# Optimization experiments

Hardware: AMD Instinct MI355X
Metric: run time of the kernel (lower is better)

Reference implementation:

```python
import jax, jax.numpy as jnp
import numpy as np

B, C, D, L, H, K, S, OUT = 8, 2048, 128, 3, 4, 200, 64, 24
d = D // H  # d_head = 32


def _ln(x, g, b):
    m = x.mean(-1, keepdims=True)
    v = ((x - m) ** 2).mean(-1, keepdims=True)
    return (x - m) / jnp.sqrt(v + 1e-5) * g + b


def _gelu(x):
    return jax.nn.gelu(x, approximate=False)  # torch default exact GELU


def setup_inputs() -> dict:
    key = jax.random.key(0)
    ks = iter(jax.random.split(key, 32))
    def nrm(shape, std=0.02):
        return jax.random.normal(next(ks), shape, jnp.float32) * std
    return {
        "x": jax.random.uniform(next(ks), (B, C), jnp.float32) * 5.0,
        "role_emb": nrm((C, D)),
        "filler_w": nrm((D,), 0.1),
        "qW": nrm((L, D, D), 0.05), "qb": jnp.zeros((L, D)),
        "kW": nrm((L, D, D), 0.05), "kb": jnp.zeros((L, D)),
        "vW": nrm((L, D, D), 0.05), "vb": jnp.zeros((L, D)),
        "oW": nrm((L, D, D), 0.05), "ob": jnp.zeros((L, D)),
        "relW1": nrm((L, 3 * d, d), 0.05), "relb1": jnp.zeros((L, d)),
        "relW2": nrm((L, d), 0.05), "relb2": jnp.zeros((L,)),
        "ln1_g": jnp.ones((L, D)), "ln1_b": jnp.zeros((L, D)),
        "ln2_g": jnp.ones((L, D)), "ln2_b": jnp.zeros((L, D)),
        "ffnW1": nrm((L, D, 4 * D), 0.05), "ffnb1": jnp.zeros((L, 4 * D)),
        "ffnW2": nrm((L, 4 * D, D), 0.05), "ffnb2": jnp.zeros((L, D)),
        "slots": nrm((S, D)),
        "memln_g": jnp.ones((D,)), "memln_b": jnp.zeros((D,)),
        "task_q": nrm((D,)),
        "headW": nrm((D, OUT), 0.05), "headb": jnp.zeros((OUT,)),
        "top_k": K,
    }


def _forward(x, role_emb, filler_w, qW, qb, kW, kb, vW, vb, oW, ob,
             relW1, relb1, relW2, relb2, ln1_g, ln1_b, ln2_g, ln2_b,
             ffnW1, ffnb1, ffnW2, ffnb2, slots, memln_g, memln_b,
             task_q, headW, headb, top_k):
    Bx = x.shape[0]
    x_log = jnp.log1p(jnp.maximum(x, 0.0))
    vals, idx = jax.lax.top_k(x_log, top_k)            # [B,K] top intensities
    roles = role_emb[idx]                              # [B,K,D]
    fillers = _gelu(vals[..., None] * filler_w)        # Linear(1,D,bias=False)+GELU
    b = roles * fillers                                # hadamard binding [B,K,D]
    sc_d = jnp.float32(d) ** 0.5
    for l in range(qW.shape[0]):
        q = (b @ qW[l] + qb[l]).reshape(Bx, -1, H, d).transpose(0, 2, 1, 3)
        k = (b @ kW[l] + kb[l]).reshape(Bx, -1, H, d).transpose(0, 2, 1, 3)
        v = (b @ vW[l] + vb[l]).reshape(Bx, -1, H, d).transpose(0, 2, 1, 3)
        # MLP_rel([q_i || k_j || q_i*k_j]) decomposed over the 3d input blocks
        W1q, W1k, W1i = relW1[l][:d], relW1[l][d:2 * d], relW1[l][2 * d:]
        qt = jnp.einsum('bhie,ef->bhif', q, W1q)       # [B,H,K,d]
        kt = jnp.einsum('bhje,ef->bhjf', k, W1k)       # [B,H,K,d]
        itm = jnp.einsum('bhie,bhje,ef->bhijf', q, k, W1i)  # pairwise [B,H,K,K,d]
        hrel = _gelu(qt[:, :, :, None, :] + kt[:, :, None, :, :] + itm + relb1[l])
        scores = (jnp.einsum('bhijf,f->bhij', hrel, relW2[l]) + relb2[l]) / sc_d
        attn = jax.nn.softmax(scores, axis=-1)
        o = jnp.einsum('bhij,bhjd->bhid', attn, v)
        o = o.transpose(0, 2, 1, 3).reshape(Bx, -1, D) @ oW[l] + ob[l]
        b = _ln(b + o, ln1_g[l], ln1_b[l])
        f = _gelu(b @ ffnW1[l] + ffnb1[l]) @ ffnW2[l] + ffnb2[l]
        b = _ln(b + f, ln2_g[l], ln2_b[l])
    sc_D = jnp.float32(D) ** 0.5
    ra = jax.nn.softmax(jnp.einsum('bcd,d->bc', b, task_q) / sc_D, axis=-1)
    h = jnp.einsum('bc,bcd->bd', ra, b)                # task-query readout
    ma = jax.nn.softmax(jnp.einsum('sd,bcd->bsc', slots, b) / sc_D, axis=-1)
    mem = _ln(jnp.einsum('bsc,bcd->bsd', ma, b).mean(axis=1), memln_g, memln_b)
    return (h + mem) @ headW + headb                   # [B,OUT]


def reference(x, role_emb, filler_w, qW, qb, kW, kb, vW, vb, oW, ob,
              relW1, relb1, relW2, relb2, ln1_g, ln1_b, ln2_g, ln2_b,
              ffnW1, ffnb1, ffnW2, ffnb2, slots, memln_g, memln_b,
              task_q, headW, headb, top_k):
    return _forward(x, role_emb, filler_w, qW, qb, kW, kb, vW, vb, oW, ob,
                    relW1, relb1, relW2, relb2, ln1_g, ln1_b, ln2_g, ln2_b,
                    ffnW1, ffnb1, ffnW2, ffnb2, slots, memln_g, memln_b,
                    task_q, headW, headb, top_k)
```

## Files before the change

kernel.cpp:

```cpp
#include <hip/hip_runtime.h>
#include <math.h>

#define BQ 8
#define CC 2048
#define DDIM 128
#define LLAY 3
#define HH 4
#define KK 200
#define SSLOT 64
#define OUTN 24
#define DH 32

typedef __bf16 bf16_t;
typedef __bf16 bf16x8 __attribute__((ext_vector_type(8)));
typedef float f32x4 __attribute__((ext_vector_type(4)));

__device__ __forceinline__ float fastrcp(float x) {
#if __has_builtin(__builtin_amdgcn_rcpf)
  return __builtin_amdgcn_rcpf(x);
#else
  return 1.0f / x;
#endif
}
__device__ __forceinline__ float fastexp2(float x) {
#if __has_builtin(__builtin_amdgcn_exp2f)
  return __builtin_amdgcn_exp2f(x);
#else
  return exp2f(x);
#endif
}
__device__ __forceinline__ float fgelu2(float x) {
  float s = x * x;
  float inner = fmaf(0.044715f * s, x, x);
  float e = fastexp2(inner * 2.302118610509359f);
  float r = fastrcp(1.f + e);
  return fmaf(-x, r, x);
}
__device__ __forceinline__ float egelu(float x) {
  return 0.5f * x * (1.f + erff(x * 0.7071067811865476f));
}

__global__ __launch_bounds__(256) void prep_kernel(
    const float* __restrict__ qW, const float* __restrict__ kW,
    const float* __restrict__ vW, const float* __restrict__ oW,
    const float* __restrict__ fW1, const float* __restrict__ fW2,
    bf16_t* __restrict__ wtb,
    const float* __restrict__ x, const float* __restrict__ role_emb,
    const float* __restrict__ fw, float* __restrict__ btok,
    bf16_t* __restrict__ btokbf) {
  __shared__ float Ts[64][65];
  __shared__ float svals[KK];
  __shared__ int sidx[KK];
  __shared__ int red[4];
  __shared__ int cnt;
  const int blk = blockIdx.x, tid = threadIdx.x;
  if (blk < 144) {
    const int t = blk;
    const float* src; bf16_t* dst; int N, K, k0, n0;
    if (t < 48) {
      int which = t / 12, rem = t % 12;
      int l = rem >> 2, tt = rem & 3;
      N = 128; K = 128; k0 = (tt >> 1) * 64; n0 = (tt & 1) * 64;
      src = (which == 0 ? qW : which == 1 ? kW : which == 2 ? vW : oW) + l * 16384;
      dst = wtb + which * 49152 + l * 16384;
    } else if (t < 96) {
      int t2 = t - 48, l = t2 >> 4, tt = t2 & 15;
      N = 512; K = 128; k0 = (tt >> 3) * 64; n0 = (tt & 7) * 64;
      src = fW1 + l * 65536;
      dst = wtb + 196608 + l * 65536;
    } else {
      int t3 = t - 96, l = t3 >> 4, tt = t3 & 15;
      N = 128; K = 512; k0 = (tt >> 1) * 64; n0 = (tt & 1) * 64;
      src = fW2 + l * 65536;
      dst = wtb + 393216 + l * 65536;
    }
#pragma unroll
    for (int i = 0; i < 16; ++i) {
      int u = tid + i * 256;
      int r = u >> 6, c = u & 63;
      Ts[r][c] = src[(size_t)(k0 + r) * N + n0 + c];
    }
    __syncthreads();
#pragma unroll
    for (int i = 0; i < 16; ++i) {
      int u = tid + i * 256;
      int rn = u >> 6, ck = u & 63;
      dst[(size_t)(n0 + rn) * K + k0 + ck] = (bf16_t)Ts[ck][rn];
    }
    return;
  }
  const int b = blk - 144;
  float xv[8]; unsigned xb[8];
#pragma unroll
  for (int t = 0; t < 8; t++) {
    float v = x[b * CC + t * 256 + tid];
    xv[t] = v;
    xb[t] = __float_as_uint(v);
  }
  unsigned lo = 0u, hi = 0x7f800000u;
  while (lo < hi) {
    unsigned mid = (lo + hi) >> 1;
    int c = 0;
#pragma unroll
    for (int t = 0; t < 8; t++) c += (xb[t] > mid) ? 1 : 0;
#pragma unroll
    for (int m = 1; m <= 32; m <<= 1) c += __shfl_xor(c, m);
    if ((tid & 63) == 0) red[tid >> 6] = c;
    __syncthreads();
    int ct = red[0] + red[1] + red[2] + red[3];
    __syncthreads();
    if (ct >= KK) lo = mid + 1; else hi = mid;
  }
  const unsigned thr = lo;
  if (tid == 0) cnt = 0;
  __syncthreads();
#pragma unroll
  for (int t = 0; t < 8; t++) {
    if (xb[t] > thr) {
      int p = atomicAdd(&cnt, 1);
      svals[p] = log1pf(xv[t]);
      sidx[p] = t * 256 + tid;
    }
  }
  __syncthreads();
#pragma unroll
  for (int t = 0; t < 8; t++) {
    if (xb[t] == thr) {
      int p = atomicAdd(&cnt, 1);
      if (p < KK) {
        svals[p] = log1pf(xv[t]);
        sidx[p] = t * 256 + tid;
      }
    }
  }
  __syncthreads();
  for (int u = tid; u < KK * DDIM; u += 256) {
    int dd = u & 127, t = u >> 7;
    float v = svals[t];
    float fill = egelu(v * fw[dd]);
    float val = role_emb[(size_t)sidx[t] * DDIM + dd] * fill;
    btok[(size_t)b * KK * DDIM + u] = val;
    btokbf[(size_t)b * KK * DDIM + u] = (bf16_t)val;
  }
}

__global__ __launch_bounds__(256) void qkv_mfma(const bf16_t* __restrict__ A,
    const bf16_t* __restrict__ qWt, const float* __restrict__ qb,
    const bf16_t* __restrict__ kWt, const float* __restrict__ kb,
    const bf16_t* __restrict__ vWt, const float* __restrict__ vb,
    bf16_t* __restrict__ qo, bf16_t* __restrict__ ko, bf16_t* __restrict__ vo) {
  __shared__ __align__(16) bf16_t Alds[32 * 16 * 8];
  __shared__ __align__(16) bf16_t Blds[128 * 16 * 8];
  const int tid = threadIdx.x, m0 = blockIdx.x * 32, z = blockIdx.y;
  const bf16_t* Wt; const float* bias; bf16_t* C;
  if (z == 0) { Wt = qWt; bias = qb; C = qo; }
  else if (z == 1) { Wt = kWt; bias = kb; C = ko; }
  else { Wt = vWt; bias = vb; C = vo; }
#pragma unroll
  for (int it = 0; it < 2; ++it) {
    int u = tid + it * 256;
    int row = u >> 4, kc = u & 15;
    uint4 d = *(const uint4*)(A + (size_t)(m0 + row) * 128 + kc * 8);
    *(uint4*)&Alds[(row * 16 + (kc ^ (row & 7))) * 8] = d;
  }
#pragma unroll
  for (int it = 0; it < 8; ++it) {
    int u = tid + it * 256;
    int col = u >> 4, kcb = u & 15;
    uint4 d = *(const uint4*)(Wt + (size_t)col * 128 + kcb * 8);
    *(uint4*)&Blds[(col * 16 + (kcb ^ (col & 7))) * 8] = d;
  }
  __syncthreads();
  const int w = tid >> 6, lane = tid & 63, fcol = lane & 15, g = lane >> 4;
  const int wr = w & 1, wn = w >> 1;
  f32x4 acc[4];
#pragma unroll
  for (int ni = 0; ni < 4; ++ni) acc[ni] = (f32x4){0.f, 0.f, 0.f, 0.f};
#pragma unroll
  for (int ks = 0; ks < 4; ++ks) {
    const int arow = 16 * wr + fcol;
    bf16x8 a = *(const bf16x8*)&Alds[(arow * 16 + ((ks * 4 + g) ^ (arow & 7))) * 8];
#pragma unroll
    for (int ni = 0; ni < 4; ++ni) {
      const int bcol = wn * 64 + ni * 16 + fcol;
      bf16x8 b = *(const bf16x8*)&Blds[(bcol * 16 + ((ks * 4 + g) ^ (bcol & 7))) * 8];
      acc[ni] = __builtin_amdgcn_mfma_f32_16x16x32_bf16(a, b, acc[ni], 0, 0, 0);
    }
  }
#pragma unroll
  for (int ni = 0; ni < 4; ++ni) {
    const int col = wn * 64 + ni * 16 + fcol;
    const float bv = bias[col];
#pragma unroll
    for (int r = 0; r < 4; ++r) {
      const int row = m0 + 16 * wr + 4 * g + r;
      C[(size_t)row * 128 + col] = (bf16_t)(acc[ni][r] + bv);
    }
  }
}

__global__ __launch_bounds__(512, 4) void rel_attn_mfma(
    const bf16_t* __restrict__ qbf, const bf16_t* __restrict__ kbf,
    const bf16_t* __restrict__ vbf,
    const float* __restrict__ W1g, const float* __restrict__ b1g,
    const float* __restrict__ w2p, bf16_t* __restrict__ o) {
  __shared__ __align__(16) bf16_t ksh[208 * 32];
  __shared__ __align__(16) bf16_t vtsh[32 * 224];
  __shared__ __align__(16) bf16_t psh[8 * 224];
  __shared__ __align__(16) bf16_t W1ki[32 * 66];
  __shared__ __align__(16) bf16_t qsh[8 * 32];
  __shared__ __align__(16) bf16_t qtshb[8 * 32];
  const int tid = threadIdx.x;
  const int bh = blockIdx.y, bb = bh >> 2, h = bh & 3;
  const int i0 = blockIdx.x * 8;
  const bf16_t* kgb = kbf + (size_t)(bb * KK) * DDIM + h * DH;
  const bf16_t* vgb = vbf + (size_t)(bb * KK) * DDIM + h * DH;
  const bf16_t* qgb = qbf + (size_t)(bb * KK) * DDIM + h * DH;
#pragma unroll
  for (int it = 0; it < 2; ++it) {
    int u = tid + it * 512;
    if (u < 832) {
      int j = u >> 2, bi = u & 3;
      uint4 d = {0u, 0u, 0u, 0u};
      if (j < KK) d = *(const uint4*)(kgb + (size_t)j * DDIM + bi * 8);
      *(uint4*)&ksh[j * 32 + (bi ^ ((j >> 1) & 3)) * 8] = d;
    }
  }
#pragma unroll
  for (int it = 0; it < 7; ++it) {
    int u = tid + it * 512;
    if (u < 3328) {
      int jp = u >> 5, f = u & 31;
      int j0 = jp * 2;
      bf16_t a0 = (j0 < KK) ? vgb[(size_t)j0 * DDIM + f] : (bf16_t)0.f;
      bf16_t a1 = (j0 + 1 < KK) ? vgb[(size_t)(j0 + 1) * DDIM + f] : (bf16_t)0.f;
      union { bf16_t h2[2]; unsigned uu; } pk;
      pk.h2[0] = a0; pk.h2[1] = a1;
      *(unsigned*)&vtsh[f * 224 + j0] = pk.uu;
    }
  }
  if (tid < 256) {
    int f = tid >> 3, cp = tid & 7;
    *(unsigned*)&vtsh[f * 224 + 208 + cp * 2] = 0u;
  }
  if (tid < 64) {
    int r = tid >> 3, cp = tid & 7;
    *(unsigned*)&psh[r * 224 + 208 + cp * 2] = 0u;
  }
#pragma unroll
  for (int it = 0; it < 4; ++it) {
    int u = tid + it * 512;
    int sel = u & 1, f = (u >> 1) & 31, e = u >> 6;
    W1ki[e * 66 + f * 2 + sel] = (bf16_t)W1g[(32 + sel * 32 + e) * 32 + f];
  }
  if (tid < 128) {
    int il = tid >> 4, ep = tid & 15;
    *(unsigned*)&qsh[il * 32 + ep * 2] =
        *(const unsigned*)(qgb + (size_t)(i0 + il) * DDIM + ep * 2);
  }
  __syncthreads();
  if (tid < 256) {
    int il = tid >> 5, f = tid & 31;
    float a = b1g[f];
#pragma unroll
    for (int e = 0; e < 32; ++e)
      a = fmaf((float)qsh[il * 32 + e], W1g[e * 32 + f], a);
    qtshb[il * 32 + f] = (bf16_t)a;
  }
  __syncthreads();
  const int w = tid >> 6, lane = tid & 63;
  const int fcol = lane & 15, g = lane >> 4;
  const float w2c = 0.17677669529663687f * 1.4426950408889634f;
  float4 w2a = *(const float4*)(w2p + 4 * g);
  float4 w2b = *(const float4*)(w2p + 16 + 4 * g);
  w2a.x *= w2c; w2a.y *= w2c; w2a.z *= w2c; w2a.w *= w2c;
  w2b.x *= w2c; w2b.y *= w2c; w2b.z *= w2c; w2b.w *= w2c;
  {
    const int il = w;
    bf16x8 qv8 = *(const bf16x8*)&qsh[il * 32 + g * 8];
    bf16x8 bw0, bw1;
#pragma unroll
    for (int e8 = 0; e8 < 8; ++e8) {
      int e = g * 8 + e8;
      float qe = (float)qv8[e8];
      union { unsigned u; bf16_t h[2]; } k0_, k1_;
      k0_.u = *(const unsigned*)&W1ki[e * 66 + fcol * 2];
      k1_.u = *(const unsigned*)&W1ki[e * 66 + (fcol + 16) * 2];
      bw0[e8] = (bf16_t)fmaf(qe, (float)k0_.h[1], (float)k0_.h[0]);
      bw1[e8] = (bf16_t)fmaf(qe, (float)k1_.h[1], (float)k1_.h[0]);
    }
    const bf16_t* qtp = &qtshb[il * 32];
    const f32x4 cin0 = {(float)qtp[4 * g + 0], (float)qtp[4 * g + 1],
                        (float)qtp[4 * g + 2], (float)qtp[4 * g + 3]};
    const f32x4 cin1 = {(float)qtp[16 + 4 * g + 0], (float)qtp[16 + 4 * g + 1],
                        (float)qtp[16 + 4 * g + 2], (float)qtp[16 + 4 * g + 3]};
    float s[13];
#pragma unroll
    for (int jt = 0; jt < 13; ++jt) {
      int j = jt * 16 + fcol;
      bf16x8 af = *(const bf16x8*)&ksh[j * 32 + (g ^ ((j >> 1) & 3)) * 8];
      f32x4 acc0 = __builtin_amdgcn_mfma_f32_16x16x32_bf16(bw0, af, cin0, 0, 0, 0);
      f32x4 acc1 = __builtin_amdgcn_mfma_f32_16x16x32_bf16(bw1, af, cin1, 0, 0, 0);
      float t0 = fgelu2(acc0[0]) * w2a.x;
      t0 = fmaf(fgelu2(acc0[1]), w2a.y, t0);
      float t1 = fgelu2(acc0[2]) * w2a.z;
      t1 = fmaf(fgelu2(acc0[3]), w2a.w, t1);
      float t2 = fgelu2(acc1[0]) * w2b.x;
      t2 = fmaf(fgelu2(acc1[1]), w2b.y, t2);
      float t3 = fgelu2(acc1[2]) * w2b.z;
      t3 = fmaf(fgelu2(acc1[3]), w2b.w, t3);
      float t = (t0 + t1) + (t2 + t3);
      t += __shfl_xor(t, 16);
      t += __shfl_xor(t, 32);
      s[jt] = t;
    }
    if (fcol >= 8) s[12] = -1e30f;
    float m = s[0];
#pragma unroll
    for (int jt = 1; jt < 13; ++jt) m = fmaxf(m, s[jt]);
    m = fmaxf(m, __shfl_xor(m, 1));
    m = fmaxf(m, __shfl_xor(m, 2));
    m = fmaxf(m, __shfl_xor(m, 4));
    m = fmaxf(m, __shfl_xor(m, 8));
    float l = 0.f;
#pragma unroll
    for (int jt = 0; jt < 13; ++jt) {
      float p = fastexp2(s[jt] - m);
      s[jt] = p;
      l += p;
    }
    l += __shfl_xor(l, 1);
    l += __shfl_xor(l, 2);
    l += __shfl_xor(l, 4);
    l += __shfl_xor(l, 8);
    const float inv = fastrcp(l);
    if (g == 0) {
#pragma unroll
      for (int jt = 0; jt < 13; ++jt)
        psh[il * 224 + jt * 16 + fcol] = (bf16_t)(s[jt] * inv);
    }
  }
  __syncthreads();
  if (w < 2) {
    f32x4 acc = {0.f, 0.f, 0.f, 0.f};
#pragma unroll
    for (int ks = 0; ks < 7; ++ks) {
      bf16x8 ap;
      if (fcol < 8) ap = *(const bf16x8*)&psh[fcol * 224 + ks * 32 + g * 8];
      else { bf16x8 z = {}; ap = z; }
      bf16x8 bv = *(const bf16x8*)&vtsh[(w * 16 + fcol) * 224 + ks * 32 + g * 8];
      acc = __builtin_amdgcn_mfma_f32_16x16x32_bf16(ap, bv, acc, 0, 0, 0);
    }
    if (g < 2) {
#pragma unroll
      for (int r = 0; r < 4; ++r) {
        int i = i0 + g * 4 + r;
        o[(size_t)(bb * KK + i) * DDIM + h * DH + w * 16 + fcol] = (bf16_t)acc[r];
      }
    }
  }
}

__global__ __launch_bounds__(512) void tail_fused(const bf16_t* __restrict__ obufbf,
    const bf16_t* __restrict__ oWt, const float* __restrict__ ob,
    const float* __restrict__ ln1g, const float* __restrict__ ln1b,
    const bf16_t* __restrict__ W1t, const float* __restrict__ b1,
    const bf16_t* __restrict__ W2t, const float* __restrict__ b2,
    const float* __restrict__ ln2g, const float* __restrict__ ln2b,
    float* __restrict__ btok, bf16_t* __restrict__ btokbf,
    const bf16_t* __restrict__ nqWt, const float* __restrict__ nqb,
    const bf16_t* __restrict__ nkWt, const float* __restrict__ nkb,
    const bf16_t* __restrict__ nvWt, const float* __restrict__ nvb,
    bf16_t* __restrict__ nqo, bf16_t* __restrict__ nko, bf16_t* __restrict__ nvo) {
  __shared__ __align__(16) bf16_t Alds[16 * 16 * 8];
  __shared__ __align__(16) bf16_t Blds[128 * 16 * 8];
  __shared__ __align__(16) bf16_t Hlds[16 * 512];
  __shared__ float lnredS[16][8], lnredQ[16][8];
  const int tid = threadIdx.x, m0 = blockIdx.x * 16;
  const int w = tid >> 6, lane = tid & 63, fcol = lane & 15, g = lane >> 4;
  const int cb = w * 16;
  const int arow = fcol;
  if (tid < 256) {
    int row = tid >> 4, kc = tid & 15;
    uint4 d = *(const uint4*)(obufbf + (size_t)(m0 + row) * 128 + kc * 8);
    *(uint4*)&Alds[(row * 16 + (kc ^ (row & 7))) * 8] = d;
  }
#pragma unroll
  for (int it = 0; it < 4; ++it) {
    int u = tid + it * 512;
    int col = u >> 4, kcb = u & 15;
    uint4 d = *(const uint4*)(oWt + (size_t)col * 128 + kcb * 8);
    *(uint4*)&Blds[(col * 16 + (kcb ^ (col & 7))) * 8] = d;
  }
  __syncthreads();
  f32x4 acc = {0.f, 0.f, 0.f, 0.f};
#pragma unroll
  for (int ks = 0; ks < 4; ++ks) {
    bf16x8 a = *(const bf16x8*)&Alds[(arow * 16 + ((ks * 4 + g) ^ (arow & 7))) * 8];
    const int bcol = cb + fcol;
    bf16x8 b = *(const bf16x8*)&Blds[(bcol * 16 + ((ks * 4 + g) ^ (bcol & 7))) * 8];
    acc = __builtin_amdgcn_mfma_f32_16x16x32_bf16(a, b, acc, 0, 0, 0);
  }
  float lnr[4];
  {
    float s_[4], q_[4];
    const int col = cb + fcol;
    const float bv = ob[col];
#pragma unroll
    for (int r = 0; r < 4; ++r) {
      const int row = m0 + 4 * g + r;
      float val = acc[r] + bv + btok[(size_t)row * 128 + col];
      lnr[r] = val;
      s_[r] = val; q_[r] = val * val;
    }
#pragma unroll
    for (int m = 1; m <= 8; m <<= 1)
#pragma unroll
      for (int r = 0; r < 4; ++r) {
        s_[r] += __shfl_xor(s_[r], m); q_[r] += __shfl_xor(q_[r], m);
      }
    if (fcol == 0) {
#pragma unroll
      for (int r = 0; r < 4; ++r) {
        lnredS[4 * g + r][w] = s_[r];
        lnredQ[4 * g + r][w] = q_[r];
      }
    }
    __syncthreads();
    float mean[4], rs[4];
#pragma unroll
    for (int r = 0; r < 4; ++r) {
      const int rl = 4 * g + r;
      float S = 0.f, Q = 0.f;
#pragma unroll
      for (int ww = 0; ww < 8; ++ww) { S += lnredS[rl][ww]; Q += lnredQ[rl][ww]; }
      mean[r] = S * (1.f / 128.f);
      rs[r] = rsqrtf(Q * (1.f / 128.f) - mean[r] * mean[r] + 1e-5f);
    }
    const float gv = ln1g[col], bv2 = ln1b[col];
#pragma unroll
    for (int r = 0; r < 4; ++r) {
      float v2 = (lnr[r] - mean[r]) * rs[r] * gv + bv2;
      lnr[r] = v2;
      const int rowL = 4 * g + r;
      Alds[(rowL * 16 + ((col >> 3) ^ (rowL & 7))) * 8 + (col & 7)] = (bf16_t)v2;
    }
  }
  __syncthreads();
  for (int nc = 0; nc < 4; ++nc) {
#pragma unroll
    for (int it = 0; it < 4; ++it) {
      int u = tid + it * 512;
      int col = u >> 4, kcb = u & 15;
      uint4 d = *(const uint4*)(W1t + (size_t)(nc * 128 + col) * 128 + kcb * 8);
      *(uint4*)&Blds[(col * 16 + (kcb ^ (col & 7))) * 8] = d;
    }
    __syncthreads();
    f32x4 a1 = {0.f, 0.f, 0.f, 0.f};
#pragma unroll
    for (int ks = 0; ks < 4; ++ks) {
      bf16x8 a = *(const bf16x8*)&Alds[(arow * 16 + ((ks * 4 + g) ^ (arow & 7))) * 8];
      const int bcol = cb + fcol;
      bf16x8 b = *(const bf16x8*)&Blds[(bcol * 16 + ((ks * 4 + g) ^ (bcol & 7))) * 8];
      a1 = __builtin_amdgcn_mfma_f32_16x16x32_bf16(a, b, a1, 0, 0, 0);
    }
    {
      const int c = nc * 128 + cb + fcol;
      const float bv = b1[c];
      const int kb = c >> 3, within = c & 7;
#pragma unroll
      for (int r = 0; r < 4; ++r) {
        const int row = 4 * g + r;
        const int kbs = kb ^ (row & 7);
        Hlds[row * 512 + kbs * 8 + within] = (bf16_t)egelu(a1[r] + bv);
      }
    }
    __syncthreads();
  }
  f32x4 acc2 = {0.f, 0.f, 0.f, 0.f};
  for (int kc = 0; kc < 4; ++kc) {
#pragma unroll
    for (int it = 0; it < 4; ++it) {
      int u = tid + it * 512;
      int col = u >> 4, kcb = u & 15;
      uint4 d = *(const uint4*)(W2t + (size_t)col * 512 + kc * 128 + kcb * 8);
      *(uint4*)&Blds[(col * 16 + (kcb ^ (col & 7))) * 8] = d;
    }
    __syncthreads();
#pragma unroll
    for (int ks = 0; ks < 4; ++ks) {
      const int kb = kc * 16 + ks * 4 + g;
      const int kbs = kb ^ (arow & 7);
      bf16x8 a = *(const bf16x8*)&Hlds[arow * 512 + kbs * 8];
      const int bcol = cb + fcol;
      bf16x8 b = *(const bf16x8*)&Blds[(bcol * 16 + ((ks * 4 + g) ^ (bcol & 7))) * 8];
      acc2 = __builtin_amdgcn_mfma_f32_16x16x32_bf16(a, b, acc2, 0, 0, 0);
    }
    __syncthreads();
  }
  {
    float s_[4], q_[4];
    const int col = cb + fcol;
    const float bv = b2[col];
#pragma unroll
    for (int r = 0; r < 4; ++r) {
      float val = acc2[r] + bv + lnr[r];
      lnr[r] = val;
      s_[r] = val; q_[r] = val * val;
    }
#pragma unroll
    for (int m = 1; m <= 8; m <<= 1)
#pragma unroll
      for (int r = 0; r < 4; ++r) {
        s_[r] += __shfl_xor(s_[r], m); q_[r] += __shfl_xor(q_[r], m);
      }
    if (fcol == 0) {
#pragma unroll
      for (int r = 0; r < 4; ++r) {
        lnredS[4 * g + r][w] = s_[r];
        lnredQ[4 * g + r][w] = q_[r];
      }
    }
    __syncthreads();
    float mean[4], rs[4];
#pragma unroll
    for (int r = 0; r < 4; ++r) {
      const int rl = 4 * g + r;
      float S = 0.f, Q = 0.f;
#pragma unroll
      for (int ww = 0; ww < 8; ++ww) { S += lnredS[rl][ww]; Q += lnredQ[rl][ww]; }
      mean[r] = S * (1.f / 128.f);
      rs[r] = rsqrtf(Q * (1.f / 128.f) - mean[r] * mean[r] + 1e-5f);
    }
    const float gv = ln2g[col], bv2 = ln2b[col];
#pragma unroll
    for (int r = 0; r < 4; ++r) {
      const int row = m0 + 4 * g + r;
      float oval = (lnr[r] - mean[r]) * rs[r] * gv + bv2;
      btok[(size_t)row * 128 + col] = oval;
      btokbf[(size_t)row * 128 + col] = (bf16_t)oval;
      if (nqWt) {
        const int rowL = 4 * g + r;
        Alds[(rowL * 16 + ((col >> 3) ^ (rowL & 7))) * 8 + (col & 7)] = (bf16_t)oval;
      }
    }
  }
  if (nqWt) {
    __syncthreads();
    const bf16_t* Ws[3] = {nqWt, nkWt, nvWt};
    const float* bs[3] = {nqb, nkb, nvb};
    bf16_t* Cs[3] = {nqo, nko, nvo};
    for (int zz = 0; zz < 3; ++zz) {
      const bf16_t* Wt = Ws[zz];
#pragma unroll
      for (int it = 0; it < 4; ++it) {
        int u = tid + it * 512;
        int col = u >> 4, kcb = u & 15;
        uint4 d = *(const uint4*)(Wt + (size_t)col * 128 + kcb * 8);
        *(uint4*)&Blds[(col * 16 + (kcb ^ (col & 7))) * 8] = d;
      }
      __syncthreads();
      f32x4 aq = {0.f, 0.f, 0.f, 0.f};
#pragma unroll
      for (int ks = 0; ks < 4; ++ks) {
        bf16x8 a = *(const bf16x8*)&Alds[(arow * 16 + ((ks * 4 + g) ^ (arow & 7))) * 8];
        const int bcol = cb + fcol;
        bf16x8 b = *(const bf16x8*)&Blds[(bcol * 16 + ((ks * 4 + g) ^ (bcol & 7))) * 8];
        aq = __builtin_amdgcn_mfma_f32_16x16x32_bf16(a, b, aq, 0, 0, 0);
      }
      const float bv = bs[zz][cb + fcol];
      bf16_t* C = Cs[zz];
#pragma unroll
      for (int r = 0; r < 4; ++r) {
        const int row = m0 + 4 * g + r;
        C[(size_t)row * 128 + cb + fcol] = (bf16_t)(aq[r] + bv);
      }
      __syncthreads();
    }
  }
}

__global__ __launch_bounds__(256) void readout_fused(const float* __restrict__ B,
    const bf16_t* __restrict__ Bbf, const float* __restrict__ slots,
    const float* __restrict__ task_q, const float* __restrict__ memg,
    const float* __restrict__ membt, const float* __restrict__ headW,
    const float* __restrict__ headb, float* __restrict__ out) {
  __shared__ __align__(16) bf16_t Ssh[64 * 16 * 8];
  __shared__ __align__(16) bf16_t Bsh[208 * 128];
  __shared__ float wcsh[4][208];
  __shared__ __align__(16) float tq[128];
  __shared__ float ras[KK];
  __shared__ float wc[208];
  __shared__ float red1[4], red2[4];
  __shared__ float hv2[256], mv2[256];
  __shared__ float hv[128], mv[128], rv[128];
  __shared__ float stats[2];
  const int b = blockIdx.x, tid = threadIdx.x;
  const int w = tid >> 6, lane = tid & 63, fcol = lane & 15, g = lane >> 4;
#pragma unroll
  for (int it = 0; it < 4; ++it) {
    int u = tid + it * 256;
    int row = u >> 4, kb = u & 15;
    const float* sp = slots + (size_t)row * 128 + kb * 8;
    bf16_t tmp[8];
#pragma unroll
    for (int e = 0; e < 8; ++e) tmp[e] = (bf16_t)sp[e];
    *(uint4*)&Ssh[(row * 16 + (kb ^ (row & 7))) * 8] = *(uint4*)tmp;
  }
#pragma unroll
  for (int it = 0; it < 13; ++it) {
    int u = tid + it * 256;
    int c = u >> 4, kb = u & 15;
    uint4 d = {0u, 0u, 0u, 0u};
    if (c < KK) d = *(const uint4*)(Bbf + (size_t)(b * KK + c) * 128 + kb * 8);
    *(uint4*)&Bsh[(c * 16 + (kb ^ (c & 7))) * 8] = d;
  }
  if (tid < 128) tq[tid] = task_q[tid];
  __syncthreads();
  {
    bf16x8 afr[4];
#pragma unroll
    for (int ks = 0; ks < 4; ++ks) {
      const int arow = 16 * w + fcol;
      afr[ks] = *(const bf16x8*)&Ssh[(arow * 16 + ((ks * 4 + g) ^ (arow & 7))) * 8];
    }
    f32x4 acc[13];
#pragma unroll
    for (int ct = 0; ct < 13; ++ct) {
      acc[ct] = (f32x4){0.f, 0.f, 0.f, 0.f};
#pragma unroll
      for (int ks = 0; ks < 4; ++ks) {
        const int bcol = ct * 16 + fcol;
        bf16x8 bb = *(const bf16x8*)&Bsh[(bcol * 16 + ((ks * 4 + g) ^ (bcol & 7))) * 8];
        acc[ct] = __builtin_amdgcn_mfma_f32_16x16x32_bf16(afr[ks], bb, acc[ct], 0, 0, 0);
      }
    }
    if (fcol >= 8) { acc[12][0] = -1e30f; acc[12][1] = -1e30f; acc[12][2] = -1e30f; acc[12][3] = -1e30f; }
    const float s2 = 0.08838834764831845f * 1.4426950408889634f;
    float wcp[13];
#pragma unroll
    for (int ct = 0; ct < 13; ++ct) wcp[ct] = 0.f;
#pragma unroll
    for (int r = 0; r < 4; ++r) {
      float m = acc[0][r];
#pragma unroll
      for (int ct = 1; ct < 13; ++ct) m = fmaxf(m, acc[ct][r]);
      m = fmaxf(m, __shfl_xor(m, 1));
      m = fmaxf(m, __shfl_xor(m, 2));
      m = fmaxf(m, __shfl_xor(m, 4));
      m = fmaxf(m, __shfl_xor(m, 8));
      float l = 0.f;
      float p[13];
#pragma unroll
      for (int ct = 0; ct < 13; ++ct) {
        p[ct] = fastexp2((acc[ct][r] - m) * s2);
        l += p[ct];
      }
      l += __shfl_xor(l, 1);
      l += __shfl_xor(l, 2);
      l += __shfl_xor(l, 4);
      l += __shfl_xor(l, 8);
      const float inv = fastrcp(l);
#pragma unroll
      for (int ct = 0; ct < 13; ++ct) wcp[ct] = fmaf(p[ct], inv, wcp[ct]);
    }
#pragma unroll
    for (int ct = 0; ct < 13; ++ct) {
      wcp[ct] += __shfl_xor(wcp[ct], 16);
      wcp[ct] += __shfl_xor(wcp[ct], 32);
      if (g == 0) wcsh[w][ct * 16 + fcol] = wcp[ct];
    }
  }
  float sc = -1e30f;
  if (tid < KK) {
    const float* br = B + (size_t)(b * KK + tid) * DDIM;
    float a = 0.f;
#pragma unroll
    for (int d4 = 0; d4 < 32; d4++) {
      float4 bb = *(const float4*)(br + d4 * 4);
      float4 ss = *(const float4*)(tq + d4 * 4);
      a += bb.x * ss.x + bb.y * ss.y + bb.z * ss.z + bb.w * ss.w;
    }
    sc = a * 0.08838834764831845f;
  }
  float mx = sc;
#pragma unroll
  for (int m = 1; m <= 32; m <<= 1) mx = fmaxf(mx, __shfl_xor(mx, m));
  if ((tid & 63) == 0) red1[tid >> 6] = mx;
  __syncthreads();
  mx = fmaxf(fmaxf(red1[0], red1[1]), fmaxf(red1[2], red1[3]));
  float p = (tid < KK) ? __expf(sc - mx) : 0.f;
  float sm = p;
#pragma unroll
  for (int m = 1; m <= 32; m <<= 1) sm += __shfl_xor(sm, m);
  if ((tid & 63) == 0) red2[tid >> 6] = sm;
  __syncthreads();
  sm = red2[0] + red2[1] + red2[2] + red2[3];
  if (tid < KK) ras[tid] = p / sm;
  if (tid < 208)
    wc[tid] = (wcsh[0][tid] + wcsh[1][tid] + wcsh[2][tid] + wcsh[3][tid]) * (1.f / 64.f);
  __syncthreads();
  {
    const int d = tid & 127, half = tid >> 7;
    float hd = 0.f, md = 0.f;
    const float* Bb = B + ((size_t)b * KK + half * 100) * DDIM + d;
    const float* rp = ras + half * 100;
    const float* wp = wc + half * 100;
#pragma unroll 2
    for (int c = 0; c < 100; ++c) {
      float bv = Bb[(size_t)c * DDIM];
      hd = fmaf(rp[c], bv, hd);
      md = fmaf(wp[c], bv, md);
    }
    hv2[tid] = hd; mv2[tid] = md;
  }
  __syncthreads();
  if (tid < 128) {
    hv[tid] = hv2[tid] + hv2[tid + 128];
    mv[tid] = mv2[tid] + mv2[tid + 128];
  }
  __syncthreads();
  if (tid < 64) {
    float x0 = mv[tid], x1 = mv[tid + 64];
    float s = x0 + x1, qq = x0 * x0 + x1 * x1;
#pragma unroll
    for (int m = 1; m <= 32; m <<= 1) { s += __shfl_xor(s, m); qq += __shfl_xor(qq, m); }
    if (tid == 0) { stats[0] = s; stats[1] = qq; }
  }
  __syncthreads();
  float mean = stats[0] * (1.f / 128.f);
  float var = stats[1] * (1.f / 128.f) - mean * mean;
  float rs = rsqrtf(var + 1e-5f);
  if (tid < 128) rv[tid] = hv[tid] + (mv[tid] - mean) * rs * memg[tid] + membt[tid];
  __syncthreads();
  if (tid < OUTN) {
    float a = headb[tid];
    for (int dd = 0; dd < 128; dd++) a = fmaf(rv[dd], headW[dd * OUTN + tid], a);
    out[b * OUTN + tid] = a;
  }
}

extern "C" void kernel_launch(void* const* d_in, const int* in_sizes, int n_in,
                              void* d_out, int out_size, void* d_ws, size_t ws_size,
                              hipStream_t stream) {
  (void)in_sizes; (void)n_in; (void)out_size; (void)ws_size;
  const float* x        = (const float*)d_in[0];
  const float* role_emb = (const float*)d_in[1];
  const float* filler_w = (const float*)d_in[2];
  const float* qW = (const float*)d_in[3];
  const float* qb = (const float*)d_in[4];
  const float* kW = (const float*)d_in[5];
  const float* kb = (const float*)d_in[6];
  const float* vW = (const float*)d_in[7];
  const float* vb = (const float*)d_in[8];
  const float* oW = (const float*)d_in[9];
  const float* ob = (const float*)d_in[10];
  const float* relW1 = (const float*)d_in[11];
  const float* relb1 = (const float*)d_in[12];
  const float* relW2 = (const float*)d_in[13];
  const float* relb2 = (const float*)d_in[14];
  const float* ln1g = (const float*)d_in[15];
  const float* ln1b = (const float*)d_in[16];
  const float* ln2g = (const float*)d_in[17];
  const float* ln2b = (const float*)d_in[18];
  const float* fW1 = (const float*)d_in[19];
  const float* fb1 = (const float*)d_in[20];
  const float* fW2 = (const float*)d_in[21];
  const float* fb2 = (const float*)d_in[22];
  const float* slots = (const float*)d_in[23];
  const float* memg = (const float*)d_in[24];
  const float* memb = (const float*)d_in[25];
  const float* taskq = (const float*)d_in[26];
  const float* headW = (const float*)d_in[27];
  const float* headb = (const float*)d_in[28];
  float* out = (float*)d_out;
  (void)relb2;

  float* fws  = (float*)d_ws;
  float*  btok   = fws;
  bf16_t* btokbf = (bf16_t*)(fws + 204800);
  bf16_t* qbf    = (bf16_t*)(fws + 307200);
  bf16_t* kbf    = (bf16_t*)(fws + 409600);
  bf16_t* vbf    = (bf16_t*)(fws + 512000);
  bf16_t* obufbf = (bf16_t*)(fws + 614400);
  bf16_t* wtb    = (bf16_t*)(fws + 716800);
  bf16_t* qWt = wtb, *kWt = wtb + 49152, *vWt = wtb + 98304, *oWt = wtb + 147456;
  bf16_t* fW1t = wtb + 196608, *fW2t = wtb + 393216;

  prep_kernel<<<152, 256, 0, stream>>>(qW, kW, vW, oW, fW1, fW2, wtb,
      x, role_emb, filler_w, btok, btokbf);
  qkv_mfma<<<dim3(50, 3), 256, 0, stream>>>(btokbf,
      qWt, qb, kWt, kb, vWt, vb, qbf, kbf, vbf);
  for (int l = 0; l < LLAY; l++) {
    rel_attn_mfma<<<dim3(25, 32), 512, 0, stream>>>(qbf, kbf, vbf,
        relW1 + l * 3072, relb1 + l * 32, relW2 + l * 32, obufbf);
    const bool nx = (l + 1 < LLAY);
    tail_fused<<<100, 512, 0, stream>>>(obufbf, oWt + l * 16384, ob + l * 128,
        ln1g + l * 128, ln1b + l * 128, fW1t + l * 65536, fb1 + l * 512,
        fW2t + l * 65536, fb2 + l * 128, ln2g + l * 128, ln2b + l * 128,
        btok, btokbf,
        nx ? qWt + (l + 1) * 16384 : (const bf16_t*)nullptr,
        nx ? qb + (l + 1) * 128 : (const float*)nullptr,
        nx ? kWt + (l + 1) * 16384 : (const bf16_t*)nullptr,
        nx ? kb + (l + 1) * 128 : (const float*)nullptr,
        nx ? vWt + (l + 1) * 16384 : (const bf16_t*)nullptr,
        nx ? vb + (l + 1) * 128 : (const float*)nullptr,
        qbf, kbf, vbf);
  }
  readout_fused<<<8, 256, 0, stream>>>(btok, btokbf, slots, taskq,
      memg, memb, headW, headb, out);
}
```

Baseline: 196.0 us.

## Use ballot top-k search, raise occupancy hints, widen readout block to 1024

The top-k threshold search now counts with wave ballots and popcount, and double-buffers its reduction slots so one barrier per iteration is dropped. The rel_attn and tail kernels get higher min-blocks launch bounds, which caps registers to allow more resident waves. The readout kernel moves to 1024 threads per block, splitting the weighted-sum reduction over 8 slices instead of 2, with the softmax restructured around the extra threads. The risks are register spills from the tighter launch bounds and extra barriers and shared-memory traffic in the readout.

After: 293.1 us. 49.6% more time.

```diff
diff --git a/kernel.cpp b/kernel.cpp
--- a/kernel.cpp
+++ b/kernel.cpp
@@ -51,7 +51,7 @@
   __shared__ float Ts[64][65];
   __shared__ float svals[KK];
   __shared__ int sidx[KK];
-  __shared__ int red[4];
+  __shared__ int redbuf[2][4];
   __shared__ int cnt;
   const int blk = blockIdx.x, tid = threadIdx.x;
   if (blk < 144) {
@@ -90,6 +90,7 @@
     return;
   }
   const int b = blk - 144;
+  const int w = tid >> 6, lane = tid & 63;
   float xv[8]; unsigned xb[8];
 #pragma unroll
   for (int t = 0; t < 8; t++) {
@@ -98,18 +99,18 @@
     xb[t] = __float_as_uint(v);
   }
   unsigned lo = 0u, hi = 0x7f800000u;
+  int itn = 0;
   while (lo < hi) {
     unsigned mid = (lo + hi) >> 1;
     int c = 0;
 #pragma unroll
-    for (int t = 0; t < 8; t++) c += (xb[t] > mid) ? 1 : 0;
-#pragma unroll
-    for (int m = 1; m <= 32; m <<= 1) c += __shfl_xor(c, m);
-    if ((tid & 63) == 0) red[tid >> 6] = c;
+    for (int t = 0; t < 8; t++) c += __popcll(__ballot(xb[t] > mid));
+    if (lane == 0) redbuf[itn & 1][w] = c;
     __syncthreads();
-    int ct = red[0] + red[1] + red[2] + red[3];
-    __syncthreads();
+    int ct = redbuf[itn & 1][0] + redbuf[itn & 1][1] +
+             redbuf[itn & 1][2] + redbuf[itn & 1][3];
     if (ct >= KK) lo = mid + 1; else hi = mid;
+    ++itn;
   }
   const unsigned thr = lo;
   if (tid == 0) cnt = 0;
@@ -199,7 +200,7 @@
   }
 }
 
-__global__ __launch_bounds__(512, 4) void rel_attn_mfma(
+__global__ __launch_bounds__(512, 8) void rel_attn_mfma(
     const bf16_t* __restrict__ qbf, const bf16_t* __restrict__ kbf,
     const bf16_t* __restrict__ vbf,
     const float* __restrict__ W1g, const float* __restrict__ b1g,
@@ -361,7 +362,7 @@
   }
 }
 
-__global__ __launch_bounds__(512) void tail_fused(const bf16_t* __restrict__ obufbf,
+__global__ __launch_bounds__(512, 6) void tail_fused(const bf16_t* __restrict__ obufbf,
     const bf16_t* __restrict__ oWt, const float* __restrict__ ob,
     const float* __restrict__ ln1g, const float* __restrict__ ln1b,
     const bf16_t* __restrict__ W1t, const float* __restrict__ b1,
@@ -580,7 +581,7 @@
   }
 }
 
-__global__ __launch_bounds__(256) void readout_fused(const float* __restrict__ B,
+__global__ __launch_bounds__(1024) void readout_fused(const float* __restrict__ B,
     const bf16_t* __restrict__ Bbf, const float* __restrict__ slots,
     const float* __restrict__ task_q, const float* __restrict__ memg,
     const float* __restrict__ membt, const float* __restrict__ headW,
@@ -592,14 +593,13 @@
   __shared__ float ras[KK];
   __shared__ float wc[208];
   __shared__ float red1[4], red2[4];
-  __shared__ float hv2[256], mv2[256];
+  __shared__ float hv2[1024], mv2[1024];
   __shared__ float hv[128], mv[128], rv[128];
   __shared__ float stats[2];
   const int b = blockIdx.x, tid = threadIdx.x;
   const int w = tid >> 6, lane = tid & 63, fcol = lane & 15, g = lane >> 4;
-#pragma unroll
-  for (int it = 0; it < 4; ++it) {
-    int u = tid + it * 256;
+  {
+    int u = tid;
     int row = u >> 4, kb = u & 15;
     const float* sp = slots + (size_t)row * 128 + kb * 8;
     bf16_t tmp[8];
@@ -608,16 +608,18 @@
     *(uint4*)&Ssh[(row * 16 + (kb ^ (row & 7))) * 8] = *(uint4*)tmp;
   }
 #pragma unroll
-  for (int it = 0; it < 13; ++it) {
-    int u = tid + it * 256;
-    int c = u >> 4, kb = u & 15;
-    uint4 d = {0u, 0u, 0u, 0u};
-    if (c < KK) d = *(const uint4*)(Bbf + (size_t)(b * KK + c) * 128 + kb * 8);
-    *(uint4*)&Bsh[(c * 16 + (kb ^ (c & 7))) * 8] = d;
+  for (int it = 0; it < 4; ++it) {
+    int u = tid + it * 1024;
+    if (u < 3328) {
+      int c = u >> 4, kb = u & 15;
+      uint4 d = {0u, 0u, 0u, 0u};
+      if (c < KK) d = *(const uint4*)(Bbf + (size_t)(b * KK + c) * 128 + kb * 8);
+      *(uint4*)&Bsh[(c * 16 + (kb ^ (c & 7))) * 8] = d;
+    }
   }
   if (tid < 128) tq[tid] = task_q[tid];
   __syncthreads();
-  {
+  if (w < 4) {
     bf16x8 afr[4];
 #pragma unroll
     for (int ks = 0; ks < 4; ++ks) {
@@ -671,43 +673,54 @@
       if (g == 0) wcsh[w][ct * 16 + fcol] = wcp[ct];
     }
   }
-  float sc = -1e30f;
+  if (tid < 256) {
+    float sc = -1e30f;
+    if (tid < KK) {
+      const float* br = B + (size_t)(b * KK + tid) * DDIM;
+      float a = 0.f;
+#pragma unroll
+      for (int d4 = 0; d4 < 32; d4++) {
+        float4 bb = *(const float4*)(br + d4 * 4);
+        float4 ss = *(const float4*)(tq + d4 * 4);
+        a += bb.x * ss.x + bb.y * ss.y + bb.z * ss.z + bb.w * ss.w;
+      }
+      sc = a * 0.08838834764831845f;
+    }
+    float mx = sc;
+#pragma unroll
+    for (int m = 1; m <= 32; m <<= 1) mx = fmaxf(mx, __shfl_xor(mx, m));
+    if (lane == 0) red1[w] = mx;
+    __threadfence_block();
+    ras[tid < KK ? tid : (KK - 1)] = 0.f;
+    hv2[tid] = sc;
+  }
+  __syncthreads();
+  if (tid < 256) {
+    float sc = hv2[tid];
+    float mx = fmaxf(fmaxf(red1[0], red1[1]), fmaxf(red1[2], red1[3]));
+    float p = (tid < KK) ? __expf(sc - mx) : 0.f;
+    float sm = p;
+#pragma unroll
+    for (int m = 1; m <= 32; m <<= 1) sm += __shfl_xor(sm, m);
+    if (lane == 0) red2[w] = sm;
+    hv2[tid] = p;
+  }
+  __syncthreads();
   if (tid < KK) {
-    const float* br = B + (size_t)(b * KK + tid) * DDIM;
-    float a = 0.f;
-#pragma unroll
-    for (int d4 = 0; d4 < 32; d4++) {
-      float4 bb = *(const float4*)(br + d4 * 4);
-      float4 ss = *(const float4*)(tq + d4 * 4);
-      a += bb.x * ss.x + bb.y * ss.y + bb.z * ss.z + bb.w * ss.w;
-    }
-    sc = a * 0.08838834764831845f;
-  }
-  float mx = sc;
-#pragma unroll
-  for (int m = 1; m <= 32; m <<= 1) mx = fmaxf(mx, __shfl_xor(mx, m));
-  if ((tid & 63) == 0) red1[tid >> 6] = mx;
-  __syncthreads();
-  mx = fmaxf(fmaxf(red1[0], red1[1]), fmaxf(red1[2], red1[3]));
-  float p = (tid < KK) ? __expf(sc - mx) : 0.f;
-  float sm = p;
-#pragma unroll
-  for (int m = 1; m <= 32; m <<= 1) sm += __shfl_xor(sm, m);
-  if ((tid & 63) == 0) red2[tid >> 6] = sm;
-  __syncthreads();
-  sm = red2[0] + red2[1] + red2[2] + red2[3];
-  if (tid < KK) ras[tid] = p / sm;
+    float sm = red2[0] + red2[1] + red2[2] + red2[3];
+    ras[tid] = hv2[tid] / sm;
+  }
   if (tid < 208)
     wc[tid] = (wcsh[0][tid] + wcsh[1][tid] + wcsh[2][tid] + wcsh[3][tid]) * (1.f / 64.f);
   __syncthreads();
   {
-    const int d = tid & 127, half = tid >> 7;
+    const int d = tid & 127, oct = tid >> 7;
     float hd = 0.f, md = 0.f;
-    const float* Bb = B + ((size_t)b * KK + half * 100) * DDIM + d;
-    const float* rp = ras + half * 100;
-    const float* wp = wc + half * 100;
-#pragma unroll 2
-    for (int c = 0; c < 100; ++c) {
+    const float* Bb = B + ((size_t)b * KK + oct * 25) * DDIM + d;
+    const float* rp = ras + oct * 25;
+    const float* wp = wc + oct * 25;
+#pragma unroll 5
+    for (int c = 0; c < 25; ++c) {
       float bv = Bb[(size_t)c * DDIM];
       hd = fmaf(rp[c], bv, hd);
       md = fmaf(wp[c], bv, md);
@@ -716,8 +729,13 @@
   }
   __syncthreads();
   if (tid < 128) {
-    hv[tid] = hv2[tid] + hv2[tid + 128];
-    mv[tid] = mv2[tid] + mv2[tid + 128];
+    float hsum = 0.f, msum = 0.f;
+#pragma unroll
+    for (int o2 = 0; o2 < 8; ++o2) {
+      hsum += hv2[tid + 128 * o2];
+      msum += mv2[tid + 128 * o2];
+    }
+    hv[tid] = hsum; mv[tid] = msum;
   }
   __syncthreads();
   if (tid < 64) {
@@ -807,6 +825,6 @@
         nx ? vb + (l + 1) * 128 : (const float*)nullptr,
         qbf, kbf, vbf);
   }
-  readout_fused<<<8, 256, 0, stream>>>(btok, btokbf, slots, taskq,
+  readout_fused<<<8, 1024, 0, stream>>>(btok, btokbf, slots, taskq,
       memg, memb, headW, headb, out);
 }
```
